# Performance work log

Hardware: AMD Instinct MI355X
Metric: run time of the kernel (lower is better)

The kernel has to match this reference:

```python
import math
import jax, jax.numpy as jnp
import numpy as np

DIM = 1024
NUM_HEADS = 16
HEAD_DIM = DIM // NUM_HEADS
SCALE = HEAD_DIM ** -0.5
ROPE_BASE = 10000.0


def _rope(x):
    # x: [b, h, t, d]; rotate-half RoPE as in the torch module
    b, h, t, d = x.shape
    half = d // 2
    freqs = jnp.exp(-math.log(ROPE_BASE) * jnp.arange(half, dtype=jnp.float32) / half)
    pos = jnp.arange(t, dtype=jnp.float32)
    angles = pos[:, None] * freqs[None, :]          # [t, half]
    sin = jnp.sin(angles)[None, None, :, :]
    cos = jnp.cos(angles)[None, None, :, :]
    x1, x2 = x[..., :half], x[..., half:]
    return jnp.concatenate([x1 * cos - x2 * sin, x1 * sin + x2 * cos], axis=-1)


def setup_inputs() -> dict:
    key = jax.random.key(0)
    k1, k2, k3, k4 = jax.random.split(key, 4)
    b, t = 2, 2048
    x = jax.random.normal(k1, (b, t, DIM), dtype=jnp.float32)
    # nn.Linear(dim, 3*dim, bias=False): store as [in, out] for x @ W
    w_qkv = jax.random.normal(k2, (DIM, 3 * DIM), dtype=jnp.float32) * (DIM ** -0.5)
    w_proj = jax.random.normal(k3, (DIM, DIM), dtype=jnp.float32) * (DIM ** -0.5)
    b_proj = jax.random.normal(k4, (DIM,), dtype=jnp.float32) * 0.02
    return {"x": x, "w_qkv": w_qkv, "w_proj": w_proj, "b_proj": b_proj}


def reference(x, w_qkv, w_proj, b_proj):
    b, t, c = x.shape
    h, hd = NUM_HEADS, HEAD_DIM
    qkv = (x @ w_qkv).reshape(b, t, 3, h, hd)
    qkv = jnp.transpose(qkv, (2, 0, 3, 1, 4))      # [3, b, h, t, hd]
    q, k, v = qkv[0], qkv[1], qkv[2]
    q, k = _rope(q), _rope(k)
    attn = jnp.einsum('bhqd,bhkd->bhqk', q, k) * SCALE
    causal_mask = jnp.triu(jnp.ones((t, t), dtype=bool), k=1)
    attn = jnp.where(causal_mask[None, None], -jnp.inf, attn)
    attn = jax.nn.softmax(attn, axis=-1)
    out = jnp.einsum('bhqk,bhkd->bhqd', attn, v)
    out = jnp.transpose(out, (0, 2, 1, 3)).reshape(b, t, c)
    return out @ w_proj + b_proj
```

## Files before the change

kernel.cpp:

```cpp
#include <hip/hip_runtime.h>
#include <math.h>

typedef unsigned short u16;
typedef unsigned int u32;
typedef __bf16 bfrag8 __attribute__((ext_vector_type(8)));
typedef float f32x4 __attribute__((ext_vector_type(4)));

#define B_ 2
#define T_ 2048
#define H_ 16
#define D_ 64
#define C_ 1024
#define NQKV_ 3072

#define MFMA_BF16(a, b, c) __builtin_amdgcn_mfma_f32_16x16x32_bf16((a), (b), (c), 0, 0, 0)

__device__ __forceinline__ u16 f2bf(float f) {
  u32 u = __builtin_bit_cast(u32, f);
  u += 0x7fffu + ((u >> 16) & 1u);
  return (u16)(u >> 16);
}

__device__ __forceinline__ void load_lds16(const u16* gp, u16* lp) {
  __builtin_amdgcn_global_load_lds(
      (const __attribute__((address_space(1))) u32*)(const void*)gp,
      (__attribute__((address_space(3))) u32*)(void*)lp, 16, 0, 0);
}

__global__ __launch_bounds__(256) void convert_x(const float* __restrict__ src,
                                                 u16* __restrict__ dst) {
  size_t i = ((size_t)blockIdx.x * 256 + threadIdx.x) * 8;
  const float* s = src + i;
  float4 a = *(const float4*)s, b = *(const float4*)(s + 4);
  union { uint4 v; u16 h[8]; } t;
  t.h[0] = f2bf(a.x); t.h[1] = f2bf(a.y); t.h[2] = f2bf(a.z); t.h[3] = f2bf(a.w);
  t.h[4] = f2bf(b.x); t.h[5] = f2bf(b.y); t.h[6] = f2bf(b.z); t.h[7] = f2bf(b.w);
  *(uint4*)(dst + i) = t.v;
}

__global__ __launch_bounds__(256) void transpose_w(const float* __restrict__ src,
                                                   u16* __restrict__ dst, int K, int N) {
  __shared__ u16 tile[64][65];
  int bx = blockIdx.x * 64;
  int by = blockIdx.y * 64;
  for (int idx = threadIdx.x; idx < 4096; idx += 256) {
    int r = idx >> 6, c = idx & 63;
    tile[r][c] = f2bf(src[(size_t)(by + r) * N + bx + c]);
  }
  __syncthreads();
  for (int idx = threadIdx.x; idx < 4096; idx += 256) {
    int r = idx >> 6, c = idx & 63;
    dst[(size_t)(bx + r) * K + by + c] = tile[c][r];
  }
}

__global__ __launch_bounds__(256) void gemm_qkv_rope(const u16* __restrict__ X,
                                                     const u16* __restrict__ WT,
                                                     u16* __restrict__ qb,
                                                     u16* __restrict__ kb,
                                                     u16* __restrict__ vb) {
  const int K = C_;
  __shared__ __align__(16) u16 As[2][128 * 32];
  __shared__ __align__(16) u16 Bs[2][128 * 32];
  int tid = threadIdx.x;
  int lane = tid & 63, wave = tid >> 6;
  int quad = lane >> 4, lr = lane & 15;
  int m0 = blockIdx.y * 128, n0 = blockIdx.x * 128;
  int wrow = (wave >> 1) * 64, wcol = (wave & 1) * 64;
  int r0 = wave * 32;
  int srow = lane >> 2, skc = (lane & 3) * 8;

  f32x4 zero = {0.f, 0.f, 0.f, 0.f};
  f32x4 acc[4][4];
#pragma unroll
  for (int i = 0; i < 4; i++)
#pragma unroll
    for (int j = 0; j < 4; j++) acc[i][j] = zero;

  const u16* ga0 = X + (size_t)(m0 + r0 + srow) * K + skc;
  const u16* ga1 = X + (size_t)(m0 + r0 + 16 + srow) * K + skc;
  const u16* gb0 = WT + (size_t)(n0 + r0 + srow) * K + skc;
  const u16* gb1 = WT + (size_t)(n0 + r0 + 16 + srow) * K + skc;

  load_lds16(ga0, &As[0][r0 * 32]);
  load_lds16(ga1, &As[0][(r0 + 16) * 32]);
  load_lds16(gb0, &Bs[0][r0 * 32]);
  load_lds16(gb1, &Bs[0][(r0 + 16) * 32]);

  int buf = 0;
  for (int k0 = 0; k0 < K; k0 += 32) {
    __syncthreads();
    if (k0 + 32 < K) {
      load_lds16(ga0 + k0 + 32, &As[buf ^ 1][r0 * 32]);
      load_lds16(ga1 + k0 + 32, &As[buf ^ 1][(r0 + 16) * 32]);
      load_lds16(gb0 + k0 + 32, &Bs[buf ^ 1][r0 * 32]);
      load_lds16(gb1 + k0 + 32, &Bs[buf ^ 1][(r0 + 16) * 32]);
    }
    bfrag8 af[4], bfr[4];
#pragma unroll
    for (int i = 0; i < 4; i++)
      af[i] = *(const bfrag8*)&As[buf][(wrow + i * 16 + lr) * 32 + quad * 8];
#pragma unroll
    for (int j = 0; j < 4; j++)
      bfr[j] = *(const bfrag8*)&Bs[buf][(wcol + j * 16 + lr) * 32 + quad * 8];
#pragma unroll
    for (int i = 0; i < 4; i++)
#pragma unroll
      for (int j = 0; j < 4; j++) acc[i][j] = MFMA_BF16(af[i], bfr[j], acc[i][j]);
    buf ^= 1;
  }

  int colbase = n0 + wcol;
  int which = colbase >> 10;
  int h = (colbase & 1023) >> 6;
  u16* dst = which == 0 ? qb : (which == 1 ? kb : vb);
  float sc0 = (which == 0) ? 0.125f : 1.0f;
  float fr0 = __expf(-0.28782313662425574f * (float)lr);
  float fr1 = __expf(-0.28782313662425574f * (float)(16 + lr));
#pragma unroll
  for (int i = 0; i < 4; i++) {
#pragma unroll
    for (int r = 0; r < 4; r++) {
      int m = m0 + wrow + i * 16 + quad * 4 + r;
      int b = m >> 11, tt = m & 2047;
      size_t base = ((size_t)(b * H_ + h) * T_ + tt) * D_;
      if (which < 2) {
        float sn, cs;
        __sincosf((float)tt * fr0, &sn, &cs);
        dst[base + lr] = f2bf((acc[i][0][r] * cs - acc[i][2][r] * sn) * sc0);
        dst[base + lr + 32] = f2bf((acc[i][0][r] * sn + acc[i][2][r] * cs) * sc0);
        __sincosf((float)tt * fr1, &sn, &cs);
        dst[base + 16 + lr] = f2bf((acc[i][1][r] * cs - acc[i][3][r] * sn) * sc0);
        dst[base + 48 + lr] = f2bf((acc[i][1][r] * sn + acc[i][3][r] * cs) * sc0);
      } else {
#pragma unroll
        for (int j = 0; j < 4; j++) dst[base + j * 16 + lr] = f2bf(acc[i][j][r]);
      }
    }
  }
}

__global__ __launch_bounds__(256) void transpose_v(const u16* __restrict__ v,
                                                   u16* __restrict__ vt) {
  __shared__ u16 tile[64][72];
  int t0 = blockIdx.x * 64;
  int bh = blockIdx.y;
  const u16* src = v + (size_t)bh * T_ * D_;
  u16* dst = vt + (size_t)bh * D_ * T_;
  for (int idx = threadIdx.x; idx < 512; idx += 256) {
    int r = idx >> 3, c8 = (idx & 7) * 8;
    *(uint4*)&tile[r][c8] = *(const uint4*)(src + (size_t)(t0 + r) * D_ + c8);
  }
  __syncthreads();
  for (int idx = threadIdx.x; idx < 512; idx += 256) {
    int d = idx >> 3, t8 = (idx & 7) * 8;
    union { uint4 u; u16 s[8]; } p;
#pragma unroll
    for (int e = 0; e < 8; e++) p.s[e] = tile[t8 + e][d];
    *(uint4*)(dst + (size_t)d * T_ + t0 + t8) = p.u;
  }
}

__global__ __launch_bounds__(256) void attn_k(const u16* __restrict__ qb,
                                              const u16* __restrict__ kb,
                                              const u16* __restrict__ vtb,
                                              u16* __restrict__ ob) {
  __shared__ __align__(16) u16 Ks[2][64 * 64];
  __shared__ __align__(16) u16 Vt[2][64 * 64];
  __shared__ __align__(16) u16 Pst[4][16 * 72];
  int tid = threadIdx.x;
  int lane = tid & 63, wave = tid >> 6;
  int quad = lane >> 4, lr = lane & 15;
  int i = blockIdx.x;
  int bq = 31 - (i >> 5);
  int bh = i & 31;
  int b = bh >> 4, h = bh & 15;
  const u16* Q = qb + (size_t)bh * T_ * D_;
  const u16* Kp = kb + (size_t)bh * T_ * D_;
  const u16* Vp = vtb + (size_t)bh * D_ * T_;
  int qr0 = bq * 64 + wave * 16;
  int r0 = wave * 16;
  int sr = lane >> 3;
  int sc = (((lane & 7) ^ (sr & 7)) * 8);

  int koff0 = ((quad ^ (lr & 7)) << 3);
  int koff1 = (((4 | quad) ^ (lr & 7)) << 3);

  bfrag8 qf[2];
#pragma unroll
  for (int ks = 0; ks < 2; ks++)
    qf[ks] = *(const bfrag8*)(Q + (size_t)(qr0 + lr) * D_ + ks * 32 + quad * 8);

  f32x4 zero = {0.f, 0.f, 0.f, 0.f};
  f32x4 o[4];
#pragma unroll
  for (int nn = 0; nn < 4; nn++) o[nn] = zero;
  float psum = 0.f;

  const u16* gk = Kp + (size_t)(r0 + sr) * D_ + sc;
  const u16* gv = Vp + (size_t)(r0 + sr) * T_ + sc;
  int niter = bq + 1;

  load_lds16(gk, &Ks[0][r0 * 64]);
  load_lds16(gk + (size_t)8 * D_, &Ks[0][(r0 + 8) * 64]);
  load_lds16(gv, &Vt[0][r0 * 64]);
  load_lds16(gv + (size_t)8 * T_, &Vt[0][(r0 + 8) * 64]);

  int buf = 0;
  int qloc = wave * 16 + lr;
  for (int it = 0; it < niter; it++) {
    __syncthreads();
    if (it + 1 < niter) {
      int tkn = (it + 1) * 64;
      load_lds16(gk + (size_t)tkn * D_, &Ks[buf ^ 1][r0 * 64]);
      load_lds16(gk + (size_t)(tkn + 8) * D_, &Ks[buf ^ 1][(r0 + 8) * 64]);
      load_lds16(gv + tkn, &Vt[buf ^ 1][r0 * 64]);
      load_lds16(gv + (size_t)8 * T_ + tkn, &Vt[buf ^ 1][(r0 + 8) * 64]);
    }
    const u16* ks_ = Ks[buf];
    const u16* vt_ = Vt[buf];

    f32x4 s[4];
#pragma unroll
    for (int j = 0; j < 4; j++) s[j] = zero;
#pragma unroll
    for (int j = 0; j < 4; j++) {
      bfrag8 kf0 = *(const bfrag8*)&ks_[(j * 16 + lr) * 64 + koff0];
      bfrag8 kf1 = *(const bfrag8*)&ks_[(j * 16 + lr) * 64 + koff1];
      s[j] = MFMA_BF16(kf0, qf[0], s[j]);
      s[j] = MFMA_BF16(kf1, qf[1], s[j]);
    }

    bool edge = (it == bq);
#pragma unroll
    for (int j = 0; j < 4; j++) {
      float p[4];
#pragma unroll
      for (int r = 0; r < 4; r++) {
        float e = __expf(s[j][r]);
        if (edge) {
          int kvloc = j * 16 + quad * 4 + r;
          e = (kvloc <= qloc) ? e : 0.f;
        }
        p[r] = e;
        psum += e;
      }
      u32 u0 = __builtin_bit_cast(u32, p[0]) + 0x8000u;
      u32 u1 = __builtin_bit_cast(u32, p[1]) + 0x8000u;
      u32 u2 = __builtin_bit_cast(u32, p[2]) + 0x8000u;
      u32 u3 = __builtin_bit_cast(u32, p[3]) + 0x8000u;
      uint2 pk;
      pk.x = (u0 >> 16) | (u1 & 0xffff0000u);
      pk.y = (u2 >> 16) | (u3 & 0xffff0000u);
      *(uint2*)&Pst[wave][lr * 72 + j * 16 + quad * 4] = pk;
    }

#pragma unroll
    for (int ks = 0; ks < 2; ks++) {
      bfrag8 pf = *(const bfrag8*)&Pst[wave][lr * 72 + ks * 32 + quad * 8];
      int ko = ks ? koff1 : koff0;
#pragma unroll
      for (int nn = 0; nn < 4; nn++) {
        bfrag8 vf = *(const bfrag8*)&vt_[(nn * 16 + lr) * 64 + ko];
        o[nn] = MFMA_BF16(pf, vf, o[nn]);
      }
    }
    buf ^= 1;
  }

  float l = psum;
  l += __shfl_xor(l, 16, 64);
  l += __shfl_xor(l, 32, 64);
  float linv = 1.0f / l;

#pragma unroll
  for (int r = 0; r < 4; r++) {
    float lrec = __shfl(linv, quad * 4 + r, 64);
    int row = qr0 + quad * 4 + r;
#pragma unroll
    for (int nn = 0; nn < 4; nn++)
      ob[(size_t)(b * T_ + row) * C_ + h * 64 + nn * 16 + lr] = f2bf(o[nn][r] * lrec);
  }
}

__global__ __launch_bounds__(256) void gemm_proj(const u16* __restrict__ A,
                                                 const u16* __restrict__ WT,
                                                 const float* __restrict__ bias,
                                                 float* __restrict__ out) {
  const int K = C_;
  __shared__ __align__(16) u16 As[2][64 * 32];
  __shared__ __align__(16) u16 Bs[2][128 * 32];
  int tid = threadIdx.x;
  int lane = tid & 63, wave = tid >> 6;
  int quad = lane >> 4, lr = lane & 15;
  int m0 = blockIdx.y * 64, n0 = blockIdx.x * 128;
  int wcol = wave * 32;
  int srow = lane >> 2, skc = (lane & 3) * 8;

  f32x4 zero = {0.f, 0.f, 0.f, 0.f};
  f32x4 acc[4][2];
#pragma unroll
  for (int i = 0; i < 4; i++)
#pragma unroll
    for (int j = 0; j < 2; j++) acc[i][j] = zero;

  const u16* ga = A + (size_t)(m0 + wave * 16 + srow) * K + skc;
  const u16* gb0 = WT + (size_t)(n0 + wave * 32 + srow) * K + skc;
  const u16* gb1 = WT + (size_t)(n0 + wave * 32 + 16 + srow) * K + skc;

  load_lds16(ga, &As[0][wave * 16 * 32]);
  load_lds16(gb0, &Bs[0][wave * 32 * 32]);
  load_lds16(gb1, &Bs[0][(wave * 32 + 16) * 32]);

  int buf = 0;
  for (int k0 = 0; k0 < K; k0 += 32) {
    __syncthreads();
    if (k0 + 32 < K) {
      load_lds16(ga + k0 + 32, &As[buf ^ 1][wave * 16 * 32]);
      load_lds16(gb0 + k0 + 32, &Bs[buf ^ 1][wave * 32 * 32]);
      load_lds16(gb1 + k0 + 32, &Bs[buf ^ 1][(wave * 32 + 16) * 32]);
    }
    bfrag8 af[4], bfr[2];
#pragma unroll
    for (int i = 0; i < 4; i++)
      af[i] = *(const bfrag8*)&As[buf][(i * 16 + lr) * 32 + quad * 8];
#pragma unroll
    for (int j = 0; j < 2; j++)
      bfr[j] = *(const bfrag8*)&Bs[buf][(wcol + j * 16 + lr) * 32 + quad * 8];
#pragma unroll
    for (int i = 0; i < 4; i++)
#pragma unroll
      for (int j = 0; j < 2; j++) acc[i][j] = MFMA_BF16(af[i], bfr[j], acc[i][j]);
    buf ^= 1;
  }

#pragma unroll
  for (int i = 0; i < 4; i++)
#pragma unroll
    for (int r = 0; r < 4; r++) {
      int m = m0 + i * 16 + quad * 4 + r;
#pragma unroll
      for (int j = 0; j < 2; j++) {
        int n = n0 + wcol + j * 16 + lr;
        out[(size_t)m * C_ + n] = acc[i][j][r] + bias[n];
      }
    }
}

extern "C" void kernel_launch(void* const* d_in, const int* in_sizes, int n_in,
                              void* d_out, int out_size, void* d_ws, size_t ws_size,
                              hipStream_t stream) {
  const float* x = (const float*)d_in[0];
  const float* w_qkv = (const float*)d_in[1];
  const float* w_proj = (const float*)d_in[2];
  const float* b_proj = (const float*)d_in[3];

  char* w = (char*)d_ws;
  u16* xb = (u16*)(w + 256);
  u16* vtb = xb;
  u16* regA = xb + (size_t)4096 * 1024;
  u16* wqkvT = regA;
  u16* abuf = regA;
  u16* wprojT = regA + (size_t)4096 * 1024;
  u16* qbuf = wprojT + (size_t)1024 * 1024;
  u16* kbuf = qbuf + (size_t)B_ * H_ * T_ * D_;
  u16* vbuf = kbuf + (size_t)B_ * H_ * T_ * D_;

  convert_x<<<2048, 256, 0, stream>>>(x, xb);
  transpose_w<<<dim3(NQKV_ / 64, C_ / 64), 256, 0, stream>>>(w_qkv, wqkvT, C_, NQKV_);
  transpose_w<<<dim3(C_ / 64, C_ / 64), 256, 0, stream>>>(w_proj, wprojT, C_, C_);
  gemm_qkv_rope<<<dim3(NQKV_ / 128, (B_ * T_) / 128), 256, 0, stream>>>(xb, wqkvT, qbuf, kbuf, vbuf);
  transpose_v<<<dim3(T_ / 64, B_ * H_), 256, 0, stream>>>(vbuf, vtb);
  attn_k<<<1024, 256, 0, stream>>>(qbuf, kbuf, vtb, abuf);
  gemm_proj<<<dim3(C_ / 128, (B_ * T_) / 64), 256, 0, stream>>>(abuf, wprojT, b_proj, (float*)d_out);
}
```

Measured before the change: 191.3 us.

## Enlarge QKV GEMM tile to 256x256 with swizzled LDS and phased barriers

Rewrites the QKV+RoPE GEMM to use 256x256 block tiles with BK=64, 512 threads, and an XOR-swizzled LDS layout for conflict-free fragment reads. The main loop is split into four MFMA phases separated by block barriers, with explicit vmcnt waits and raised wave priority around the MFMA phases, while the next K stage is prefetched. The goal is more data reuse per loaded byte and less LDS bank contention. The trade-off is that the grid drops to 192 blocks, fewer than the number of CUs, and each block uses much more LDS and more registers.

```diff
diff --git a/kernel.cpp b/kernel.cpp
--- a/kernel.cpp
+++ b/kernel.cpp
@@ -25,6 +25,14 @@
   __builtin_amdgcn_global_load_lds(
       (const __attribute__((address_space(1))) u32*)(const void*)gp,
       (__attribute__((address_space(3))) u32*)(void*)lp, 16, 0, 0);
+}
+
+__device__ __forceinline__ void block_barrier() {
+  __builtin_amdgcn_sched_barrier(0);
+  asm volatile("" ::: "memory");
+  __builtin_amdgcn_s_barrier();
+  asm volatile("" ::: "memory");
+  __builtin_amdgcn_sched_barrier(0);
 }
 
 __global__ __launch_bounds__(256) void convert_x(const float* __restrict__ src,
@@ -54,63 +62,109 @@
   }
 }
 
-__global__ __launch_bounds__(256) void gemm_qkv_rope(const u16* __restrict__ X,
+#define QKV_STAGE(kt, b)                                               \
+  {                                                                    \
+    _Pragma("unroll") for (int l = 0; l < 4; l++) {                    \
+      load_lds16(gA + (size_t)(l * 64) * C_ + (kt) * 64,               \
+                 &As[b][(l * 64 + wave * 8) * 64]);                    \
+      load_lds16(gB + (size_t)(l * 64) * C_ + (kt) * 64,               \
+                 &Bs[b][(l * 64 + wave * 8) * 64]);                    \
+    }                                                                  \
+  }
+
+#define QKV_LOADA(i0)                                                            \
+  {                                                                              \
+    _Pragma("unroll") for (int ii = 0; ii < 4; ii++) {                           \
+      af[ii][0] = *(const bfrag8*)&as_[(rA + ((i0) + ii) * 16) * 64 + cofs0];    \
+      af[ii][1] = *(const bfrag8*)&as_[(rA + ((i0) + ii) * 16) * 64 + cofs1];    \
+    }                                                                            \
+  }
+
+#define QKV_LOADB(j0)                                                            \
+  {                                                                              \
+    _Pragma("unroll") for (int jj = 0; jj < 2; jj++) {                           \
+      bf[jj][0] = *(const bfrag8*)&bs_[(rB + ((j0) + jj) * 16) * 64 + cofs0];    \
+      bf[jj][1] = *(const bfrag8*)&bs_[(rB + ((j0) + jj) * 16) * 64 + cofs1];    \
+    }                                                                            \
+  }
+
+#define QKV_MMA(i0, j0)                                                          \
+  {                                                                              \
+    __builtin_amdgcn_s_setprio(1);                                               \
+    _Pragma("unroll") for (int ii = 0; ii < 4; ii++)                             \
+        _Pragma("unroll") for (int jj = 0; jj < 2; jj++) {                       \
+      acc[(i0) + ii][(j0) + jj] =                                                \
+          MFMA_BF16(af[ii][0], bf[jj][0], acc[(i0) + ii][(j0) + jj]);            \
+      acc[(i0) + ii][(j0) + jj] =                                                \
+          MFMA_BF16(af[ii][1], bf[jj][1], acc[(i0) + ii][(j0) + jj]);            \
+    }                                                                            \
+    __builtin_amdgcn_s_setprio(0);                                               \
+  }
+
+__global__ __launch_bounds__(512) void gemm_qkv_rope(const u16* __restrict__ X,
                                                      const u16* __restrict__ WT,
                                                      u16* __restrict__ qb,
                                                      u16* __restrict__ kb,
                                                      u16* __restrict__ vb) {
-  const int K = C_;
-  __shared__ __align__(16) u16 As[2][128 * 32];
-  __shared__ __align__(16) u16 Bs[2][128 * 32];
+  const int NT = 16;
+  __shared__ __align__(16) u16 As[2][256 * 64];
+  __shared__ __align__(16) u16 Bs[2][256 * 64];
   int tid = threadIdx.x;
   int lane = tid & 63, wave = tid >> 6;
   int quad = lane >> 4, lr = lane & 15;
-  int m0 = blockIdx.y * 128, n0 = blockIdx.x * 128;
-  int wrow = (wave >> 1) * 64, wcol = (wave & 1) * 64;
-  int r0 = wave * 32;
-  int srow = lane >> 2, skc = (lane & 3) * 8;
+  int wm = wave >> 2, wn = wave & 3;
+  int m0 = blockIdx.y * 256, n0 = blockIdx.x * 256;
+
+  int srow = lane >> 3;
+  int schunk = (lane & 7) ^ srow;
+  const u16* gA = X + (size_t)(m0 + wave * 8 + srow) * C_ + schunk * 8;
+  const u16* gB = WT + (size_t)(n0 + wave * 8 + srow) * C_ + schunk * 8;
+
+  int rA = wm * 128 + lr;
+  int rB = wn * 64 + lr;
+  int cofs0 = (quad ^ (lr & 7)) * 8;
+  int cofs1 = ((4 | quad) ^ (lr & 7)) * 8;
 
   f32x4 zero = {0.f, 0.f, 0.f, 0.f};
-  f32x4 acc[4][4];
-#pragma unroll
-  for (int i = 0; i < 4; i++)
+  f32x4 acc[8][4];
+#pragma unroll
+  for (int i = 0; i < 8; i++)
 #pragma unroll
     for (int j = 0; j < 4; j++) acc[i][j] = zero;
 
-  const u16* ga0 = X + (size_t)(m0 + r0 + srow) * K + skc;
-  const u16* ga1 = X + (size_t)(m0 + r0 + 16 + srow) * K + skc;
-  const u16* gb0 = WT + (size_t)(n0 + r0 + srow) * K + skc;
-  const u16* gb1 = WT + (size_t)(n0 + r0 + 16 + srow) * K + skc;
-
-  load_lds16(ga0, &As[0][r0 * 32]);
-  load_lds16(ga1, &As[0][(r0 + 16) * 32]);
-  load_lds16(gb0, &Bs[0][r0 * 32]);
-  load_lds16(gb1, &Bs[0][(r0 + 16) * 32]);
-
-  int buf = 0;
-  for (int k0 = 0; k0 < K; k0 += 32) {
-    __syncthreads();
-    if (k0 + 32 < K) {
-      load_lds16(ga0 + k0 + 32, &As[buf ^ 1][r0 * 32]);
-      load_lds16(ga1 + k0 + 32, &As[buf ^ 1][(r0 + 16) * 32]);
-      load_lds16(gb0 + k0 + 32, &Bs[buf ^ 1][r0 * 32]);
-      load_lds16(gb1 + k0 + 32, &Bs[buf ^ 1][(r0 + 16) * 32]);
-    }
-    bfrag8 af[4], bfr[4];
-#pragma unroll
-    for (int i = 0; i < 4; i++)
-      af[i] = *(const bfrag8*)&As[buf][(wrow + i * 16 + lr) * 32 + quad * 8];
-#pragma unroll
-    for (int j = 0; j < 4; j++)
-      bfr[j] = *(const bfrag8*)&Bs[buf][(wcol + j * 16 + lr) * 32 + quad * 8];
-#pragma unroll
-    for (int i = 0; i < 4; i++)
-#pragma unroll
-      for (int j = 0; j < 4; j++) acc[i][j] = MFMA_BF16(af[i], bfr[j], acc[i][j]);
-    buf ^= 1;
-  }
-
-  int colbase = n0 + wcol;
+  bfrag8 af[4][2], bf[2][2];
+
+  QKV_STAGE(0, 0);
+
+#pragma unroll 1
+  for (int kt = 0; kt < NT; kt++) {
+    const u16* as_ = As[kt & 1];
+    const u16* bs_ = Bs[kt & 1];
+    if (kt + 1 < NT) {
+      QKV_STAGE(kt + 1, (kt + 1) & 1);
+      asm volatile("s_waitcnt vmcnt(8)" ::: "memory");
+      __builtin_amdgcn_sched_barrier(0);
+    } else {
+      asm volatile("s_waitcnt vmcnt(0)" ::: "memory");
+      __builtin_amdgcn_sched_barrier(0);
+    }
+    block_barrier();
+    QKV_LOADA(0);
+    QKV_LOADB(0);
+    QKV_MMA(0, 0);
+    block_barrier();
+    QKV_LOADB(2);
+    QKV_MMA(0, 2);
+    block_barrier();
+    QKV_LOADA(4);
+    QKV_MMA(4, 2);
+    block_barrier();
+    QKV_LOADB(0);
+    QKV_MMA(4, 0);
+    block_barrier();
+  }
+
+  int colbase = n0 + wn * 64;
   int which = colbase >> 10;
   int h = (colbase & 1023) >> 6;
   u16* dst = which == 0 ? qb : (which == 1 ? kb : vb);
@@ -118,10 +172,10 @@
   float fr0 = __expf(-0.28782313662425574f * (float)lr);
   float fr1 = __expf(-0.28782313662425574f * (float)(16 + lr));
 #pragma unroll
-  for (int i = 0; i < 4; i++) {
+  for (int i = 0; i < 8; i++) {
 #pragma unroll
     for (int r = 0; r < 4; r++) {
-      int m = m0 + wrow + i * 16 + quad * 4 + r;
+      int m = m0 + wm * 128 + i * 16 + quad * 4 + r;
       int b = m >> 11, tt = m & 2047;
       size_t base = ((size_t)(b * H_ + h) * T_ + tt) * D_;
       if (which < 2) {
@@ -369,7 +423,7 @@
   convert_x<<<2048, 256, 0, stream>>>(x, xb);
   transpose_w<<<dim3(NQKV_ / 64, C_ / 64), 256, 0, stream>>>(w_qkv, wqkvT, C_, NQKV_);
   transpose_w<<<dim3(C_ / 64, C_ / 64), 256, 0, stream>>>(w_proj, wprojT, C_, C_);
-  gemm_qkv_rope<<<dim3(NQKV_ / 128, (B_ * T_) / 128), 256, 0, stream>>>(xb, wqkvT, qbuf, kbuf, vbuf);
+  gemm_qkv_rope<<<dim3(NQKV_ / 256, (B_ * T_) / 256), 512, 0, stream>>>(xb, wqkvT, qbuf, kbuf, vbuf);
   transpose_v<<<dim3(T_ / 64, B_ * H_), 256, 0, stream>>>(vbuf, vtb);
   attn_k<<<1024, 256, 0, stream>>>(qbuf, kbuf, vtb, abuf);
   gemm_proj<<<dim3(C_ / 128, (B_ * T_) / 64), 256, 0, stream>>>(abuf, wprojT, b_proj, (float*)d_out);
```

Measured after the change: 195.5 us. 2.2% more time.

## Fuse x fp32-to-bf16 conversion into QKV GEMM, remap blocks, prioritize MFMA

Applied to the files above, without the earlier changes.

Drops the standalone convert_x kernel. The QKV GEMM now loads fp32 x tiles straight into LDS with an XOR swizzle and converts them to bf16 while building the MFMA fragments. It also remaps block ids so neighbouring blocks share tiles for better L2 reuse, and raises wave priority around the MFMA sections of attention. The trade is one fewer launch and no intermediate bf16 x write and read, against twice the LDS footprint and load traffic for the A operand plus extra conversion ALU work in the GEMM inner loop.

```diff
diff --git a/kernel.cpp b/kernel.cpp
--- a/kernel.cpp
+++ b/kernel.cpp
@@ -26,16 +26,10 @@
       (const __attribute__((address_space(1))) u32*)(const void*)gp,
       (__attribute__((address_space(3))) u32*)(void*)lp, 16, 0, 0);
 }
-
-__global__ __launch_bounds__(256) void convert_x(const float* __restrict__ src,
-                                                 u16* __restrict__ dst) {
-  size_t i = ((size_t)blockIdx.x * 256 + threadIdx.x) * 8;
-  const float* s = src + i;
-  float4 a = *(const float4*)s, b = *(const float4*)(s + 4);
-  union { uint4 v; u16 h[8]; } t;
-  t.h[0] = f2bf(a.x); t.h[1] = f2bf(a.y); t.h[2] = f2bf(a.z); t.h[3] = f2bf(a.w);
-  t.h[4] = f2bf(b.x); t.h[5] = f2bf(b.y); t.h[6] = f2bf(b.z); t.h[7] = f2bf(b.w);
-  *(uint4*)(dst + i) = t.v;
+__device__ __forceinline__ void load_lds16f(const float* gp, float* lp) {
+  __builtin_amdgcn_global_load_lds(
+      (const __attribute__((address_space(1))) u32*)(const void*)gp,
+      (__attribute__((address_space(3))) u32*)(void*)lp, 16, 0, 0);
 }
 
 __global__ __launch_bounds__(256) void transpose_w(const float* __restrict__ src,
@@ -54,21 +48,25 @@
   }
 }
 
-__global__ __launch_bounds__(256) void gemm_qkv_rope(const u16* __restrict__ X,
+__global__ __launch_bounds__(256) void gemm_qkv_rope(const float* __restrict__ Xf,
                                                      const u16* __restrict__ WT,
                                                      u16* __restrict__ qb,
                                                      u16* __restrict__ kb,
                                                      u16* __restrict__ vb) {
   const int K = C_;
-  __shared__ __align__(16) u16 As[2][128 * 32];
+  __shared__ __align__(16) float Asf[2][128 * 32];
   __shared__ __align__(16) u16 Bs[2][128 * 32];
   int tid = threadIdx.x;
   int lane = tid & 63, wave = tid >> 6;
   int quad = lane >> 4, lr = lane & 15;
-  int m0 = blockIdx.y * 128, n0 = blockIdx.x * 128;
+  int id = blockIdx.x + blockIdx.y * 24;
+  int nid = (id & 7) * 96 + (id >> 3);
+  int m0 = (nid / 24) * 128, n0 = (nid % 24) * 128;
   int wrow = (wave >> 1) * 64, wcol = (wave & 1) * 64;
   int r0 = wave * 32;
-  int srow = lane >> 2, skc = (lane & 3) * 8;
+  int srowB = lane >> 2, skcB = (lane & 3) * 8;
+  int srowA = lane >> 3;
+  int schA = (lane & 7) ^ srowA;
 
   f32x4 zero = {0.f, 0.f, 0.f, 0.f};
   f32x4 acc[4][4];
@@ -77,29 +75,42 @@
 #pragma unroll
     for (int j = 0; j < 4; j++) acc[i][j] = zero;
 
-  const u16* ga0 = X + (size_t)(m0 + r0 + srow) * K + skc;
-  const u16* ga1 = X + (size_t)(m0 + r0 + 16 + srow) * K + skc;
-  const u16* gb0 = WT + (size_t)(n0 + r0 + srow) * K + skc;
-  const u16* gb1 = WT + (size_t)(n0 + r0 + 16 + srow) * K + skc;
-
-  load_lds16(ga0, &As[0][r0 * 32]);
-  load_lds16(ga1, &As[0][(r0 + 16) * 32]);
+  const float* gaF = Xf + (size_t)(m0 + r0 + srowA) * K + schA * 4;
+  const u16* gb0 = WT + (size_t)(n0 + r0 + srowB) * K + skcB;
+  const u16* gb1 = WT + (size_t)(n0 + r0 + 16 + srowB) * K + skcB;
+
+  load_lds16f(gaF, &Asf[0][r0 * 32]);
+  load_lds16f(gaF + (size_t)8 * K, &Asf[0][(r0 + 8) * 32]);
+  load_lds16f(gaF + (size_t)16 * K, &Asf[0][(r0 + 16) * 32]);
+  load_lds16f(gaF + (size_t)24 * K, &Asf[0][(r0 + 24) * 32]);
   load_lds16(gb0, &Bs[0][r0 * 32]);
   load_lds16(gb1, &Bs[0][(r0 + 16) * 32]);
+
+  int ca0 = ((quad * 2) ^ (lr & 7)) * 4;
+  int ca1 = ((quad * 2 + 1) ^ (lr & 7)) * 4;
 
   int buf = 0;
   for (int k0 = 0; k0 < K; k0 += 32) {
     __syncthreads();
     if (k0 + 32 < K) {
-      load_lds16(ga0 + k0 + 32, &As[buf ^ 1][r0 * 32]);
-      load_lds16(ga1 + k0 + 32, &As[buf ^ 1][(r0 + 16) * 32]);
+      load_lds16f(gaF + k0 + 32, &Asf[buf ^ 1][r0 * 32]);
+      load_lds16f(gaF + (size_t)8 * K + k0 + 32, &Asf[buf ^ 1][(r0 + 8) * 32]);
+      load_lds16f(gaF + (size_t)16 * K + k0 + 32, &Asf[buf ^ 1][(r0 + 16) * 32]);
+      load_lds16f(gaF + (size_t)24 * K + k0 + 32, &Asf[buf ^ 1][(r0 + 24) * 32]);
       load_lds16(gb0 + k0 + 32, &Bs[buf ^ 1][r0 * 32]);
       load_lds16(gb1 + k0 + 32, &Bs[buf ^ 1][(r0 + 16) * 32]);
     }
     bfrag8 af[4], bfr[4];
 #pragma unroll
-    for (int i = 0; i < 4; i++)
-      af[i] = *(const bfrag8*)&As[buf][(wrow + i * 16 + lr) * 32 + quad * 8];
+    for (int i = 0; i < 4; i++) {
+      const float* ar = &Asf[buf][(wrow + i * 16 + lr) * 32];
+      float4 a0 = *(const float4*)(ar + ca0);
+      float4 a1 = *(const float4*)(ar + ca1);
+      bfrag8 f;
+      f[0] = (__bf16)a0.x; f[1] = (__bf16)a0.y; f[2] = (__bf16)a0.z; f[3] = (__bf16)a0.w;
+      f[4] = (__bf16)a1.x; f[5] = (__bf16)a1.y; f[6] = (__bf16)a1.z; f[7] = (__bf16)a1.w;
+      af[i] = f;
+    }
 #pragma unroll
     for (int j = 0; j < 4; j++)
       bfr[j] = *(const bfrag8*)&Bs[buf][(wcol + j * 16 + lr) * 32 + quad * 8];
@@ -223,6 +234,7 @@
     f32x4 s[4];
 #pragma unroll
     for (int j = 0; j < 4; j++) s[j] = zero;
+    __builtin_amdgcn_s_setprio(1);
 #pragma unroll
     for (int j = 0; j < 4; j++) {
       bfrag8 kf0 = *(const bfrag8*)&ks_[(j * 16 + lr) * 64 + koff0];
@@ -230,6 +242,7 @@
       s[j] = MFMA_BF16(kf0, qf[0], s[j]);
       s[j] = MFMA_BF16(kf1, qf[1], s[j]);
     }
+    __builtin_amdgcn_s_setprio(0);
 
     bool edge = (it == bq);
 #pragma unroll
@@ -255,6 +268,7 @@
       *(uint2*)&Pst[wave][lr * 72 + j * 16 + quad * 4] = pk;
     }
 
+    __builtin_amdgcn_s_setprio(1);
 #pragma unroll
     for (int ks = 0; ks < 2; ks++) {
       bfrag8 pf = *(const bfrag8*)&Pst[wave][lr * 72 + ks * 32 + quad * 8];
@@ -265,6 +279,7 @@
         o[nn] = MFMA_BF16(pf, vf, o[nn]);
       }
     }
+    __builtin_amdgcn_s_setprio(0);
     buf ^= 1;
   }
 
@@ -356,9 +371,8 @@
   const float* b_proj = (const float*)d_in[3];
 
   char* w = (char*)d_ws;
-  u16* xb = (u16*)(w + 256);
-  u16* vtb = xb;
-  u16* regA = xb + (size_t)4096 * 1024;
+  u16* vtb = (u16*)(w + 256);
+  u16* regA = vtb + (size_t)4096 * 1024;
   u16* wqkvT = regA;
   u16* abuf = regA;
   u16* wprojT = regA + (size_t)4096 * 1024;
@@ -366,10 +380,9 @@
   u16* kbuf = qbuf + (size_t)B_ * H_ * T_ * D_;
   u16* vbuf = kbuf + (size_t)B_ * H_ * T_ * D_;
 
-  convert_x<<<2048, 256, 0, stream>>>(x, xb);
   transpose_w<<<dim3(NQKV_ / 64, C_ / 64), 256, 0, stream>>>(w_qkv, wqkvT, C_, NQKV_);
   transpose_w<<<dim3(C_ / 64, C_ / 64), 256, 0, stream>>>(w_proj, wprojT, C_, C_);
-  gemm_qkv_rope<<<dim3(NQKV_ / 128, (B_ * T_) / 128), 256, 0, stream>>>(xb, wqkvT, qbuf, kbuf, vbuf);
+  gemm_qkv_rope<<<dim3(NQKV_ / 128, (B_ * T_) / 128), 256, 0, stream>>>(x, wqkvT, qbuf, kbuf, vbuf);
   transpose_v<<<dim3(T_ / 64, B_ * H_), 256, 0, stream>>>(vbuf, vtb);
   attn_k<<<1024, 256, 0, stream>>>(qbuf, kbuf, vtb, abuf);
   gemm_proj<<<dim3(C_ / 128, (B_ * T_) / 64), 256, 0, stream>>>(abuf, wprojT, b_proj, (float*)d_out);
```

Result: slower. 233.2 us (+21.9%).

## Triple-buffer LDS in QKV and projection GEMMs with explicit vmcnt waits

Applied to the files above, without the earlier changes.

Both GEMM kernels move from double to triple buffering of the A/B LDS tiles. Prefetch runs two k-steps ahead and uses partial s_waitcnt vmcnt counts instead of a full __syncthreads drain, with sched_barrier fences around a raw s_barrier. The aim is to hide more global-to-LDS latency behind MFMA work. In exchange, LDS use per block grows by half, which may lower occupancy, and correctness now depends on the hand-set vmcnt values being right.

```diff
diff --git a/kernel.cpp b/kernel.cpp
--- a/kernel.cpp
+++ b/kernel.cpp
@@ -25,6 +25,14 @@
   __builtin_amdgcn_global_load_lds(
       (const __attribute__((address_space(1))) u32*)(const void*)gp,
       (__attribute__((address_space(3))) u32*)(void*)lp, 16, 0, 0);
+}
+
+__device__ __forceinline__ void block_barrier() {
+  __builtin_amdgcn_sched_barrier(0);
+  asm volatile("" ::: "memory");
+  __builtin_amdgcn_s_barrier();
+  asm volatile("" ::: "memory");
+  __builtin_amdgcn_sched_barrier(0);
 }
 
 __global__ __launch_bounds__(256) void convert_x(const float* __restrict__ src,
@@ -60,8 +68,9 @@
                                                      u16* __restrict__ kb,
                                                      u16* __restrict__ vb) {
   const int K = C_;
-  __shared__ __align__(16) u16 As[2][128 * 32];
-  __shared__ __align__(16) u16 Bs[2][128 * 32];
+  const int NTI = 32;
+  __shared__ __align__(16) u16 As[3][128 * 32];
+  __shared__ __align__(16) u16 Bs[3][128 * 32];
   int tid = threadIdx.x;
   int lane = tid & 63, wave = tid >> 6;
   int quad = lane >> 4, lr = lane & 15;
@@ -86,28 +95,41 @@
   load_lds16(ga1, &As[0][(r0 + 16) * 32]);
   load_lds16(gb0, &Bs[0][r0 * 32]);
   load_lds16(gb1, &Bs[0][(r0 + 16) * 32]);
-
-  int buf = 0;
-  for (int k0 = 0; k0 < K; k0 += 32) {
-    __syncthreads();
-    if (k0 + 32 < K) {
-      load_lds16(ga0 + k0 + 32, &As[buf ^ 1][r0 * 32]);
-      load_lds16(ga1 + k0 + 32, &As[buf ^ 1][(r0 + 16) * 32]);
-      load_lds16(gb0 + k0 + 32, &Bs[buf ^ 1][r0 * 32]);
-      load_lds16(gb1 + k0 + 32, &Bs[buf ^ 1][(r0 + 16) * 32]);
+  load_lds16(ga0 + 32, &As[1][r0 * 32]);
+  load_lds16(ga1 + 32, &As[1][(r0 + 16) * 32]);
+  load_lds16(gb0 + 32, &Bs[1][r0 * 32]);
+  load_lds16(gb1 + 32, &Bs[1][(r0 + 16) * 32]);
+
+  int bc = 0;
+#pragma unroll 1
+  for (int kt = 0; kt < NTI; kt++) {
+    if (kt < NTI - 1) {
+      asm volatile("s_waitcnt vmcnt(4)" ::: "memory");
+    } else {
+      asm volatile("s_waitcnt vmcnt(0)" ::: "memory");
+    }
+    __builtin_amdgcn_sched_barrier(0);
+    block_barrier();
+    if (kt < NTI - 2) {
+      int bn = bc + 2; if (bn >= 3) bn -= 3;
+      int kn = kt * 32 + 64;
+      load_lds16(ga0 + kn, &As[bn][r0 * 32]);
+      load_lds16(ga1 + kn, &As[bn][(r0 + 16) * 32]);
+      load_lds16(gb0 + kn, &Bs[bn][r0 * 32]);
+      load_lds16(gb1 + kn, &Bs[bn][(r0 + 16) * 32]);
     }
     bfrag8 af[4], bfr[4];
 #pragma unroll
     for (int i = 0; i < 4; i++)
-      af[i] = *(const bfrag8*)&As[buf][(wrow + i * 16 + lr) * 32 + quad * 8];
+      af[i] = *(const bfrag8*)&As[bc][(wrow + i * 16 + lr) * 32 + quad * 8];
 #pragma unroll
     for (int j = 0; j < 4; j++)
-      bfr[j] = *(const bfrag8*)&Bs[buf][(wcol + j * 16 + lr) * 32 + quad * 8];
+      bfr[j] = *(const bfrag8*)&Bs[bc][(wcol + j * 16 + lr) * 32 + quad * 8];
 #pragma unroll
     for (int i = 0; i < 4; i++)
 #pragma unroll
       for (int j = 0; j < 4; j++) acc[i][j] = MFMA_BF16(af[i], bfr[j], acc[i][j]);
-    buf ^= 1;
+    bc = (bc == 2) ? 0 : bc + 1;
   }
 
   int colbase = n0 + wcol;
@@ -288,8 +310,9 @@
                                                  const float* __restrict__ bias,
                                                  float* __restrict__ out) {
   const int K = C_;
-  __shared__ __align__(16) u16 As[2][64 * 32];
-  __shared__ __align__(16) u16 Bs[2][128 * 32];
+  const int NTI = 32;
+  __shared__ __align__(16) u16 As[3][64 * 32];
+  __shared__ __align__(16) u16 Bs[3][128 * 32];
   int tid = threadIdx.x;
   int lane = tid & 63, wave = tid >> 6;
   int quad = lane >> 4, lr = lane & 15;
@@ -311,27 +334,39 @@
   load_lds16(ga, &As[0][wave * 16 * 32]);
   load_lds16(gb0, &Bs[0][wave * 32 * 32]);
   load_lds16(gb1, &Bs[0][(wave * 32 + 16) * 32]);
-
-  int buf = 0;
-  for (int k0 = 0; k0 < K; k0 += 32) {
-    __syncthreads();
-    if (k0 + 32 < K) {
-      load_lds16(ga + k0 + 32, &As[buf ^ 1][wave * 16 * 32]);
-      load_lds16(gb0 + k0 + 32, &Bs[buf ^ 1][wave * 32 * 32]);
-      load_lds16(gb1 + k0 + 32, &Bs[buf ^ 1][(wave * 32 + 16) * 32]);
+  load_lds16(ga + 32, &As[1][wave * 16 * 32]);
+  load_lds16(gb0 + 32, &Bs[1][wave * 32 * 32]);
+  load_lds16(gb1 + 32, &Bs[1][(wave * 32 + 16) * 32]);
+
+  int bc = 0;
+#pragma unroll 1
+  for (int kt = 0; kt < NTI; kt++) {
+    if (kt < NTI - 1) {
+      asm volatile("s_waitcnt vmcnt(3)" ::: "memory");
+    } else {
+      asm volatile("s_waitcnt vmcnt(0)" ::: "memory");
+    }
+    __builtin_amdgcn_sched_barrier(0);
+    block_barrier();
+    if (kt < NTI - 2) {
+      int bn = bc + 2; if (bn >= 3) bn -= 3;
+      int kn = kt * 32 + 64;
+      load_lds16(ga + kn, &As[bn][wave * 16 * 32]);
+      load_lds16(gb0 + kn, &Bs[bn][wave * 32 * 32]);
+      load_lds16(gb1 + kn, &Bs[bn][(wave * 32 + 16) * 32]);
     }
     bfrag8 af[4], bfr[2];
 #pragma unroll
     for (int i = 0; i < 4; i++)
-      af[i] = *(const bfrag8*)&As[buf][(i * 16 + lr) * 32 + quad * 8];
+      af[i] = *(const bfrag8*)&As[bc][(i * 16 + lr) * 32 + quad * 8];
 #pragma unroll
     for (int j = 0; j < 2; j++)
-      bfr[j] = *(const bfrag8*)&Bs[buf][(wcol + j * 16 + lr) * 32 + quad * 8];
+      bfr[j] = *(const bfrag8*)&Bs[bc][(wcol + j * 16 + lr) * 32 + quad * 8];
 #pragma unroll
     for (int i = 0; i < 4; i++)
 #pragma unroll
       for (int j = 0; j < 2; j++) acc[i][j] = MFMA_BF16(af[i], bfr[j], acc[i][j]);
-    buf ^= 1;
+    bc = (bc == 2) ? 0 : bc + 1;
   }
 
 #pragma unroll
```

After: 199.2 us. +4.2%, slower.
